# Performance work log

Hardware: AMD Instinct MI355X
Metric: run time of the kernel (lower is better)

The kernel has to match this reference:

```python
import jax, jax.numpy as jnp
import numpy as np

B, C_IN, C_OUT, K, H, W = 16, 256, 512, 7, 64, 64
PAD = K // 2


def setup_inputs() -> dict:
    key = jax.random.key(0)
    k1, k2, k3 = jax.random.split(key, 3)
    x = jax.random.normal(k1, (B, C_IN, H, W), dtype=jnp.float32)
    # depthwise weight: [out_channels=C_IN, in_channels//groups=1, k, k]
    fan_dw = 1 * K * K
    dw_w = jax.random.normal(k2, (C_IN, 1, K, K), dtype=jnp.float32) * np.sqrt(2.0 / fan_dw)
    dw_b = jnp.zeros((C_IN,), dtype=jnp.float32)
    # pointwise weight: [C_OUT, C_IN, 1, 1]
    pw_w = jax.random.normal(k3, (C_OUT, C_IN, 1, 1), dtype=jnp.float32) * np.sqrt(2.0 / C_IN)
    pw_b = jnp.zeros((C_OUT,), dtype=jnp.float32)
    return {"x": x, "dw_w": dw_w, "dw_b": dw_b, "pw_w": pw_w, "pw_b": pw_b}


def reference(x, dw_w, dw_b, pw_w, pw_b):
    # Depthwise conv (groups == C_in): cross-correlation, same as the torch
    # unfold+einsum construction with zero padding k//2.
    y = jax.lax.conv_general_dilated(
        x, dw_w,
        window_strides=(1, 1),
        padding=[(PAD, PAD), (PAD, PAD)],
        feature_group_count=C_IN,
        dimension_numbers=("NCHW", "OIHW", "NCHW"),
    )
    y = y + dw_b[None, :, None, None]
    # Pointwise 1x1 conv == per-pixel GEMM over channels.
    out = jnp.einsum("bchw,oc->bohw", y, pw_w[:, :, 0, 0])
    out = out + pw_b[None, :, None, None]
    return out
```

## Files before the change

kernel.cpp:

```cpp
#include <hip/hip_runtime.h>

typedef unsigned short US;
typedef __bf16 bf16x8 __attribute__((ext_vector_type(8)));
typedef float f32x4 __attribute__((ext_vector_type(4)));

__device__ __forceinline__ US f2bf(float f) {
  union { float f; unsigned u; } v; v.f = f;
  unsigned r = v.u + 0x7fffu + ((v.u >> 16) & 1u);
  return (US)(r >> 16);
}
__device__ __forceinline__ float blo(unsigned u) {
  union { unsigned u; float f; } v; v.u = u << 16; return v.f;
}
__device__ __forceinline__ float bhi(unsigned u) {
  union { unsigned u; float f; } v; v.u = u & 0xffff0000u; return v.f;
}

__global__ __launch_bounds__(256) void k_convw(const float* __restrict__ pw,
                                               US* __restrict__ wb) {
  int i = (blockIdx.x * 256 + threadIdx.x) * 4;
  float4 v = *(const float4*)(pw + i);
  ushort4 s;
  s.x = f2bf(v.x); s.y = f2bf(v.y); s.z = f2bf(v.z); s.w = f2bf(v.w);
  *(ushort4*)(wb + i) = s;
}

__global__ __launch_bounds__(512, 4) void k_dw(const float* __restrict__ x,
                                               const float* __restrict__ dww,
                                               const float* __restrict__ dwb,
                                               US* __restrict__ y8) {
  const int bid = blockIdx.x;
  const int rg  = bid & 3;
  const int cg  = (bid >> 2) & 31;
  const int b   = bid >> 7;
  const int t   = threadIdx.x;
  const int w   = t >> 6;
  const int l   = t & 63;
  const int g   = l >> 4;
  const int cb  = l & 15;
  const int c   = __builtin_amdgcn_readfirstlane(cg * 8 + w);
  const float* xp = x + ((size_t)b * 256 + c) * 4096;

  __shared__ US xl[8][24][64];
  __shared__ US t8[8][1024];

  const int r0 = rg * 16;

  {
    const int rowl0 = l >> 3;
    const int colb  = (l & 7) * 8;
#pragma unroll
    for (int it = 0; it < 3; ++it) {
      const int rowl = it * 8 + rowl0;
      const int gr   = r0 - 3 + rowl;
      const int grc  = min(max(gr, 0), 63);
      const float* gp = xp + grc * 64 + colb;
      float4 f0 = *(const float4*)(gp);
      float4 f1 = *(const float4*)(gp + 4);
      uint4 pk;
      pk.x = ((unsigned)f2bf(f0.y) << 16) | f2bf(f0.x);
      pk.y = ((unsigned)f2bf(f0.w) << 16) | f2bf(f0.z);
      pk.z = ((unsigned)f2bf(f1.y) << 16) | f2bf(f1.x);
      pk.w = ((unsigned)f2bf(f1.w) << 16) | f2bf(f1.z);
      *(uint4*)&xl[w][rowl][colb] = pk;
    }
  }

  float wv[49];
  const float* wp = dww + c * 49;
#pragma unroll
  for (int i = 0; i < 49; ++i) wv[i] = wp[i];
  const float bias = dwb[c];

  __syncthreads();

  const int bcx  = cb * 4;
  const bool colL = (bcx >= 4);
  const bool colR = (bcx < 60);
  const int offL  = colL ? -4 : 0;
  const int offR  = colR ?  4 : 0;

  float acc[4][4];
#pragma unroll
  for (int o = 0; o < 4; ++o)
#pragma unroll
    for (int q = 0; q < 4; ++q) acc[o][q] = bias;

#pragma unroll
  for (int j = 0; j < 10; ++j) {
    const int gr = r0 + g * 4 - 3 + j;
    const bool rowOK = ((unsigned)gr < 64u);
    const US* rp = &xl[w][g * 4 + j][bcx];
    uint2 va = *(const uint2*)(rp + offL);
    uint2 vb = *(const uint2*)(rp);
    uint2 vc = *(const uint2*)(rp + offR);
    const bool okL = rowOK && colL;
    const bool okR = rowOK && colR;
    va.x = okL   ? va.x : 0u;  va.y = okL   ? va.y : 0u;
    vb.x = rowOK ? vb.x : 0u;  vb.y = rowOK ? vb.y : 0u;
    vc.x = okR   ? vc.x : 0u;  vc.y = okR   ? vc.y : 0u;
    float L[12];
    L[0] = blo(va.x); L[1]  = bhi(va.x); L[2]  = blo(va.y); L[3]  = bhi(va.y);
    L[4] = blo(vb.x); L[5]  = bhi(vb.x); L[6]  = blo(vb.y); L[7]  = bhi(vb.y);
    L[8] = blo(vc.x); L[9]  = bhi(vc.x); L[10] = blo(vc.y); L[11] = bhi(vc.y);
#pragma unroll
    for (int o = 0; o < 4; ++o) {
      if (j - o >= 0 && j - o <= 6) {
        const int kh = j - o;
#pragma unroll
        for (int kw = 0; kw < 7; ++kw) {
          const float wk = wv[kh * 7 + kw];
#pragma unroll
          for (int q = 0; q < 4; ++q)
            acc[o][q] = fmaf(L[q + kw + 1], wk, acc[o][q]);
        }
      }
    }
  }

#pragma unroll
  for (int o = 0; o < 4; ++o) {
    ushort4 s;
    s.x = f2bf(acc[o][0]); s.y = f2bf(acc[o][1]);
    s.z = f2bf(acc[o][2]); s.w = f2bf(acc[o][3]);
    *(ushort4*)&t8[w][(g * 4 + o) * 64 + bcx] = s;
  }
  __syncthreads();

  unsigned rc8[8];
#pragma unroll
  for (int c2 = 0; c2 < 8; ++c2) rc8[c2] = *(const unsigned*)&t8[c2][2 * t];
  uint4 A, B2;
  A.x  = __builtin_amdgcn_perm(rc8[1], rc8[0], 0x05040100u);
  A.y  = __builtin_amdgcn_perm(rc8[3], rc8[2], 0x05040100u);
  A.z  = __builtin_amdgcn_perm(rc8[5], rc8[4], 0x05040100u);
  A.w  = __builtin_amdgcn_perm(rc8[7], rc8[6], 0x05040100u);
  B2.x = __builtin_amdgcn_perm(rc8[1], rc8[0], 0x07060302u);
  B2.y = __builtin_amdgcn_perm(rc8[3], rc8[2], 0x07060302u);
  B2.z = __builtin_amdgcn_perm(rc8[5], rc8[4], 0x07060302u);
  B2.w = __builtin_amdgcn_perm(rc8[7], rc8[6], 0x07060302u);
  US* yb = y8 + (((size_t)b * 32 + cg) * 4096 + r0 * 64) * 8 + (size_t)t * 16;
  *(uint4*)(yb)     = A;
  *(uint4*)(yb + 8) = B2;
}

__global__ __launch_bounds__(256, 2) void k_pw(const US* __restrict__ y8,
                                               const US* __restrict__ wb,
                                               const float* __restrict__ pwb,
                                               float* __restrict__ out) {
  const int bid = blockIdx.x;
  const int s   = ((bid & 7) << 8) | (bid >> 3);
  const int b   = s >> 7;
  const int rr  = s & 127;
  const int nt  = rr >> 2;
  const int mt  = rr & 3;
  const int o0  = mt * 128;
  const int hw0 = nt * 128;

  __shared__ US lsA[2][128][72];
  __shared__ US lsB[2][128][72];
  const int tid  = threadIdx.x;
  const int lane = tid & 63;
  const int wid  = tid >> 6;
  const int wm   = wid >> 1, wn = wid & 1;
  const int strow = tid >> 3;
  const int scg   = tid & 7;
  const int bg    = tid >> 5;
  const int bl    = tid & 31;

  const f32x4 fzero = {0.f, 0.f, 0.f, 0.f};
  f32x4 acc[4][4];
#pragma unroll
  for (int m = 0; m < 4; ++m)
#pragma unroll
    for (int n = 0; n < 4; ++n) acc[m][n] = fzero;

  uint4 ra[4], rb[4];
#pragma unroll
  for (int i = 0; i < 4; ++i) {
    ra[i] = *(const uint4*)(wb + (size_t)(o0 + i * 32 + strow) * 256 + scg * 8);
    rb[i] = *(const uint4*)(y8 + ((size_t)(b * 32 + bg) * 4096 + hw0 + bl + 32 * i) * 8);
  }
#pragma unroll
  for (int i = 0; i < 4; ++i) {
    *(uint4*)&lsA[0][i * 32 + strow][scg * 8] = ra[i];
    *(uint4*)&lsB[0][bl + 32 * i][bg * 8]     = rb[i];
  }
  __syncthreads();

  for (int kt = 0; kt < 4; ++kt) {
    const int cur = kt & 1;
    if (kt < 3) {
      const int ck = (kt + 1) * 64;
#pragma unroll
      for (int i = 0; i < 4; ++i) {
        ra[i] = *(const uint4*)(wb + (size_t)(o0 + i * 32 + strow) * 256 + ck + scg * 8);
        rb[i] = *(const uint4*)(y8 + ((size_t)(b * 32 + (ck >> 3) + bg) * 4096 + hw0 + bl + 32 * i) * 8);
      }
    }
    bf16x8 af[2][4], bfr[2][4];
#pragma unroll
    for (int kk = 0; kk < 2; ++kk) {
      const int kcol = kk * 32 + (lane >> 4) * 8;
#pragma unroll
      for (int m = 0; m < 4; ++m)
        af[kk][m] = *reinterpret_cast<const bf16x8*>(&lsA[cur][wm * 64 + m * 16 + (lane & 15)][kcol]);
#pragma unroll
      for (int n = 0; n < 4; ++n)
        bfr[kk][n] = *reinterpret_cast<const bf16x8*>(&lsB[cur][wn * 64 + n * 16 + (lane & 15)][kcol]);
    }
#pragma unroll
    for (int kk = 0; kk < 2; ++kk)
#pragma unroll
      for (int m = 0; m < 4; ++m)
#pragma unroll
        for (int n = 0; n < 4; ++n)
          acc[m][n] = __builtin_amdgcn_mfma_f32_16x16x32_bf16(bfr[kk][n], af[kk][m], acc[m][n], 0, 0, 0);

    if (kt < 3) {
#pragma unroll
      for (int i = 0; i < 4; ++i) {
        *(uint4*)&lsA[cur ^ 1][i * 32 + strow][scg * 8] = ra[i];
        *(uint4*)&lsB[cur ^ 1][bl + 32 * i][bg * 8]     = rb[i];
      }
      __syncthreads();
    }
  }

#pragma unroll
  for (int m = 0; m < 4; ++m) {
    const int o  = o0 + wm * 64 + m * 16 + (lane & 15);
    const float bv = pwb[o];
    float* orow = out + (((size_t)b * 512 + o) * 4096) + hw0 + wn * 64 + (lane >> 4) * 4;
#pragma unroll
    for (int n = 0; n < 4; ++n) {
      f32x4 v = acc[m][n];
      v[0] += bv; v[1] += bv; v[2] += bv; v[3] += bv;
      *(f32x4*)(orow + n * 16) = v;
    }
  }
}

extern "C" void kernel_launch(void* const* d_in, const int* in_sizes, int n_in,
                              void* d_out, int out_size, void* d_ws, size_t ws_size,
                              hipStream_t stream) {
  const float* x   = (const float*)d_in[0];
  const float* dww = (const float*)d_in[1];
  const float* dwb = (const float*)d_in[2];
  const float* pww = (const float*)d_in[3];
  const float* pwb = (const float*)d_in[4];
  float* out = (float*)d_out;

  char* ws = (char*)d_ws;
  US* y8  = (US*)ws;
  US* wbf = (US*)(ws + 33554432);

  k_convw<<<128,  256, 0, stream>>>(pww, wbf);
  k_dw   <<<2048, 512, 0, stream>>>(x, dww, dwb, y8);
  k_pw   <<<2048, 256, 0, stream>>>(y8, wbf, pwb, out);
}
```

Measured before the change: 74.98 us.

## Process two row-blocks per depthwise block with register prefetch of second tile

The depthwise kernel now handles two 16-row slabs per block, halving the grid. It prefetches the second slab's input into registers while the first slab computes, then converts it and writes it to a second shared buffer. The aim is to hide global load latency and amortize the weight and bias loads. In exchange, shared memory and register use grow, and the launch bound drops to 2 blocks per SM. There also appears to be no barrier between writing xl[1] and reading it, which may race across waves.

```diff
diff --git a/kernel.cpp b/kernel.cpp
--- a/kernel.cpp
+++ b/kernel.cpp
@@ -25,14 +25,14 @@
   *(ushort4*)(wb + i) = s;
 }
 
-__global__ __launch_bounds__(512, 4) void k_dw(const float* __restrict__ x,
+__global__ __launch_bounds__(512, 2) void k_dw(const float* __restrict__ x,
                                                const float* __restrict__ dww,
                                                const float* __restrict__ dwb,
                                                US* __restrict__ y8) {
   const int bid = blockIdx.x;
-  const int rg  = bid & 3;
-  const int cg  = (bid >> 2) & 31;
-  const int b   = bid >> 7;
+  const int rg2 = bid & 1;
+  const int cg  = (bid >> 1) & 31;
+  const int b   = bid >> 6;
   const int t   = threadIdx.x;
   const int w   = t >> 6;
   const int l   = t & 63;
@@ -41,19 +41,24 @@
   const int c   = __builtin_amdgcn_readfirstlane(cg * 8 + w);
   const float* xp = x + ((size_t)b * 256 + c) * 4096;
 
-  __shared__ US xl[8][24][64];
-  __shared__ US t8[8][1024];
-
-  const int r0 = rg * 16;
+  __shared__ US xl[2][8][24][64];
+  __shared__ US t8[2][8][1024];
+
+  const int rowl0 = l >> 3;
+  const int colb  = (l & 7) * 8;
+
+  float wv[49];
+  const float* wp = dww + c * 49;
+#pragma unroll
+  for (int i = 0; i < 49; ++i) wv[i] = wp[i];
+  const float bias = dwb[c];
 
   {
-    const int rowl0 = l >> 3;
-    const int colb  = (l & 7) * 8;
+    const int r00 = (rg2 * 2) * 16;
 #pragma unroll
     for (int it = 0; it < 3; ++it) {
       const int rowl = it * 8 + rowl0;
-      const int gr   = r0 - 3 + rowl;
-      const int grc  = min(max(gr, 0), 63);
+      const int grc  = min(max(r00 - 3 + rowl, 0), 63);
       const float* gp = xp + grc * 64 + colb;
       float4 f0 = *(const float4*)(gp);
       float4 f1 = *(const float4*)(gp + 4);
@@ -62,17 +67,9 @@
       pk.y = ((unsigned)f2bf(f0.w) << 16) | f2bf(f0.z);
       pk.z = ((unsigned)f2bf(f1.y) << 16) | f2bf(f1.x);
       pk.w = ((unsigned)f2bf(f1.w) << 16) | f2bf(f1.z);
-      *(uint4*)&xl[w][rowl][colb] = pk;
-    }
-  }
-
-  float wv[49];
-  const float* wp = dww + c * 49;
-#pragma unroll
-  for (int i = 0; i < 49; ++i) wv[i] = wp[i];
-  const float bias = dwb[c];
-
-  __syncthreads();
+      *(uint4*)&xl[0][w][rowl][colb] = pk;
+    }
+  }
 
   const int bcx  = cb * 4;
   const bool colL = (bcx >= 4);
@@ -80,68 +77,97 @@
   const int offL  = colL ? -4 : 0;
   const int offR  = colR ?  4 : 0;
 
-  float acc[4][4];
-#pragma unroll
-  for (int o = 0; o < 4; ++o)
-#pragma unroll
-    for (int q = 0; q < 4; ++q) acc[o][q] = bias;
-
-#pragma unroll
-  for (int j = 0; j < 10; ++j) {
-    const int gr = r0 + g * 4 - 3 + j;
-    const bool rowOK = ((unsigned)gr < 64u);
-    const US* rp = &xl[w][g * 4 + j][bcx];
-    uint2 va = *(const uint2*)(rp + offL);
-    uint2 vb = *(const uint2*)(rp);
-    uint2 vc = *(const uint2*)(rp + offR);
-    const bool okL = rowOK && colL;
-    const bool okR = rowOK && colR;
-    va.x = okL   ? va.x : 0u;  va.y = okL   ? va.y : 0u;
-    vb.x = rowOK ? vb.x : 0u;  vb.y = rowOK ? vb.y : 0u;
-    vc.x = okR   ? vc.x : 0u;  vc.y = okR   ? vc.y : 0u;
-    float L[12];
-    L[0] = blo(va.x); L[1]  = bhi(va.x); L[2]  = blo(va.y); L[3]  = bhi(va.y);
-    L[4] = blo(vb.x); L[5]  = bhi(vb.x); L[6]  = blo(vb.y); L[7]  = bhi(vb.y);
-    L[8] = blo(vc.x); L[9]  = bhi(vc.x); L[10] = blo(vc.y); L[11] = bhi(vc.y);
+  float4 pfa[3], pfb[3];
+
+#pragma unroll
+  for (int h = 0; h < 2; ++h) {
+    const int r0h = (rg2 * 2 + h) * 16;
+
+    if (h == 0) {
+      const int r01 = (rg2 * 2 + 1) * 16;
+#pragma unroll
+      for (int it = 0; it < 3; ++it) {
+        const int grc = min(max(r01 - 3 + it * 8 + rowl0, 0), 63);
+        const float* gp = xp + grc * 64 + colb;
+        pfa[it] = *(const float4*)(gp);
+        pfb[it] = *(const float4*)(gp + 4);
+      }
+    } else {
+#pragma unroll
+      for (int it = 0; it < 3; ++it) {
+        const int rowl = it * 8 + rowl0;
+        uint4 pk;
+        pk.x = ((unsigned)f2bf(pfa[it].y) << 16) | f2bf(pfa[it].x);
+        pk.y = ((unsigned)f2bf(pfa[it].w) << 16) | f2bf(pfa[it].z);
+        pk.z = ((unsigned)f2bf(pfb[it].y) << 16) | f2bf(pfb[it].x);
+        pk.w = ((unsigned)f2bf(pfb[it].w) << 16) | f2bf(pfb[it].z);
+        *(uint4*)&xl[1][w][rowl][colb] = pk;
+      }
+    }
+
+    float acc[4][4];
+#pragma unroll
+    for (int o = 0; o < 4; ++o)
+#pragma unroll
+      for (int q = 0; q < 4; ++q) acc[o][q] = bias;
+
+#pragma unroll
+    for (int j = 0; j < 10; ++j) {
+      const int gr = r0h + g * 4 - 3 + j;
+      const bool rowOK = ((unsigned)gr < 64u);
+      const US* rp = &xl[h][w][g * 4 + j][bcx];
+      uint2 va = *(const uint2*)(rp + offL);
+      uint2 vb = *(const uint2*)(rp);
+      uint2 vc = *(const uint2*)(rp + offR);
+      const bool okL = rowOK && colL;
+      const bool okR = rowOK && colR;
+      va.x = okL   ? va.x : 0u;  va.y = okL   ? va.y : 0u;
+      vb.x = rowOK ? vb.x : 0u;  vb.y = rowOK ? vb.y : 0u;
+      vc.x = okR   ? vc.x : 0u;  vc.y = okR   ? vc.y : 0u;
+      float L[12];
+      L[0] = blo(va.x); L[1]  = bhi(va.x); L[2]  = blo(va.y); L[3]  = bhi(va.y);
+      L[4] = blo(vb.x); L[5]  = bhi(vb.x); L[6]  = blo(vb.y); L[7]  = bhi(vb.y);
+      L[8] = blo(vc.x); L[9]  = bhi(vc.x); L[10] = blo(vc.y); L[11] = bhi(vc.y);
+#pragma unroll
+      for (int o = 0; o < 4; ++o) {
+        if (j - o >= 0 && j - o <= 6) {
+          const int kh = j - o;
+#pragma unroll
+          for (int kw = 0; kw < 7; ++kw) {
+            const float wk = wv[kh * 7 + kw];
+#pragma unroll
+            for (int q = 0; q < 4; ++q)
+              acc[o][q] = fmaf(L[q + kw + 1], wk, acc[o][q]);
+          }
+        }
+      }
+    }
+
 #pragma unroll
     for (int o = 0; o < 4; ++o) {
-      if (j - o >= 0 && j - o <= 6) {
-        const int kh = j - o;
-#pragma unroll
-        for (int kw = 0; kw < 7; ++kw) {
-          const float wk = wv[kh * 7 + kw];
-#pragma unroll
-          for (int q = 0; q < 4; ++q)
-            acc[o][q] = fmaf(L[q + kw + 1], wk, acc[o][q]);
-        }
-      }
-    }
-  }
-
-#pragma unroll
-  for (int o = 0; o < 4; ++o) {
-    ushort4 s;
-    s.x = f2bf(acc[o][0]); s.y = f2bf(acc[o][1]);
-    s.z = f2bf(acc[o][2]); s.w = f2bf(acc[o][3]);
-    *(ushort4*)&t8[w][(g * 4 + o) * 64 + bcx] = s;
-  }
-  __syncthreads();
-
-  unsigned rc8[8];
-#pragma unroll
-  for (int c2 = 0; c2 < 8; ++c2) rc8[c2] = *(const unsigned*)&t8[c2][2 * t];
-  uint4 A, B2;
-  A.x  = __builtin_amdgcn_perm(rc8[1], rc8[0], 0x05040100u);
-  A.y  = __builtin_amdgcn_perm(rc8[3], rc8[2], 0x05040100u);
-  A.z  = __builtin_amdgcn_perm(rc8[5], rc8[4], 0x05040100u);
-  A.w  = __builtin_amdgcn_perm(rc8[7], rc8[6], 0x05040100u);
-  B2.x = __builtin_amdgcn_perm(rc8[1], rc8[0], 0x07060302u);
-  B2.y = __builtin_amdgcn_perm(rc8[3], rc8[2], 0x07060302u);
-  B2.z = __builtin_amdgcn_perm(rc8[5], rc8[4], 0x07060302u);
-  B2.w = __builtin_amdgcn_perm(rc8[7], rc8[6], 0x07060302u);
-  US* yb = y8 + (((size_t)b * 32 + cg) * 4096 + r0 * 64) * 8 + (size_t)t * 16;
-  *(uint4*)(yb)     = A;
-  *(uint4*)(yb + 8) = B2;
+      ushort4 s;
+      s.x = f2bf(acc[o][0]); s.y = f2bf(acc[o][1]);
+      s.z = f2bf(acc[o][2]); s.w = f2bf(acc[o][3]);
+      *(ushort4*)&t8[h][w][(g * 4 + o) * 64 + bcx] = s;
+    }
+    __syncthreads();
+
+    unsigned rc8[8];
+#pragma unroll
+    for (int c2 = 0; c2 < 8; ++c2) rc8[c2] = *(const unsigned*)&t8[h][c2][2 * t];
+    uint4 A, B2;
+    A.x  = __builtin_amdgcn_perm(rc8[1], rc8[0], 0x05040100u);
+    A.y  = __builtin_amdgcn_perm(rc8[3], rc8[2], 0x05040100u);
+    A.z  = __builtin_amdgcn_perm(rc8[5], rc8[4], 0x05040100u);
+    A.w  = __builtin_amdgcn_perm(rc8[7], rc8[6], 0x05040100u);
+    B2.x = __builtin_amdgcn_perm(rc8[1], rc8[0], 0x07060302u);
+    B2.y = __builtin_amdgcn_perm(rc8[3], rc8[2], 0x07060302u);
+    B2.z = __builtin_amdgcn_perm(rc8[5], rc8[4], 0x07060302u);
+    B2.w = __builtin_amdgcn_perm(rc8[7], rc8[6], 0x07060302u);
+    US* yb = y8 + (((size_t)b * 32 + cg) * 4096 + r0h * 64) * 8 + (size_t)t * 16;
+    *(uint4*)(yb)     = A;
+    *(uint4*)(yb + 8) = B2;
+  }
 }
 
 __global__ __launch_bounds__(256, 2) void k_pw(const US* __restrict__ y8,
@@ -256,6 +282,6 @@
   US* wbf = (US*)(ws + 33554432);
 
   k_convw<<<128,  256, 0, stream>>>(pww, wbf);
-  k_dw   <<<2048, 512, 0, stream>>>(x, dww, dwb, y8);
+  k_dw   <<<1024, 512, 0, stream>>>(x, dww, dwb, y8);
   k_pw   <<<2048, 256, 0, stream>>>(y8, wbf, pwb, out);
 }
```

Result: slower. 79.41 us (+5.9%).
